# Kernel optimization log

Hardware: AMD Instinct MI355X
Metric: run time of the kernel (lower is better)

## Reference

```python
import jax, jax.numpy as jnp
import numpy as np


def _l2norm(x):
    # matches torch F.normalize(p=2, dim=-1) with eps clamp
    return x / jnp.clip(jnp.linalg.norm(x, axis=-1, keepdims=True), 1e-12)


def setup_inputs() -> dict:
    key = jax.random.key(0)
    k1, k2 = jax.random.split(key)
    I, J, S, H = 32, 32, 256, 768
    return {
        "query_embs": jax.random.normal(k1, (I, S, H), dtype=jnp.float32),
        "key_embs": jax.random.normal(k2, (J, S, H), dtype=jnp.float32),
        "q_mask": jnp.ones((I, S), dtype=jnp.float32),
        "k_mask": jnp.ones((J, S), dtype=jnp.float32),
        "alpha_raw": jnp.asarray(0.5, dtype=jnp.float32),  # learned scalar param
    }


def reference(query_embs, key_embs, q_mask, k_mask, alpha_raw):
    # eval path: gumbel_temp=None, use_max=False, do_distance=True, exp_decay=True
    S = query_embs.shape[1]
    pos = jnp.arange(S)
    distance = jnp.abs(pos[:, None] - pos[None, :]).astype(jnp.float32)  # [S, S]
    alpha = jax.nn.softplus(alpha_raw)

    qn = _l2norm(query_embs)  # [I, S, H]
    kn = _l2norm(key_embs)    # [J, T, H]

    # cross similarity [I, J, S, T] with exponential distance decay
    sim = jnp.einsum('ish,jth->ijst', qn, kn) * jnp.exp(-alpha * distance)

    # valid pair mask [I, J, S, T]
    valid = q_mask[:, None, :, None] * k_mask[None, :, None, :]
    masked = sim * valid - (1.0 - valid) * 1e9

    p = jax.nn.softmax(masked, axis=-1)             # softmax over key tokens t
    agg = jnp.einsum('ijst,jth->ijsh', p, kn)       # soft-aligned key embedding
    scores = jnp.einsum('ish,ijsh->ijs', qn, agg)   # per-query-token score
    scores = scores * q_mask[:, None, :]
    denom = jnp.clip(jnp.sum(q_mask, axis=-1, keepdims=True), 1.0)  # [I, 1]
    return jnp.sum(scores, axis=-1) / denom         # [I, J]
```

## Files before the change

### kernel.cpp

```cpp
#include <hip/hip_runtime.h>

#define I_DIM 32
#define J_DIM 32
#define S_DIM 256
#define H_DIM 768
#define KC    32
#define NCH   (H_DIM / KC)
#define TILE_B 32768
#define WSQ_BYTES ((size_t)I_DIM * NCH * TILE_B)
#define WSK_BYTES ((size_t)J_DIM * NCH * TILE_B)

typedef _Float16 f16x8 __attribute__((ext_vector_type(8)));
typedef float    f32x16 __attribute__((ext_vector_type(16)));

static __device__ __forceinline__ unsigned short f16bits(_Float16 h) {
    union { _Float16 f; unsigned short u; } cv; cv.f = h; return cv.u;
}

__global__ __launch_bounds__(256) void li_split_kernel(
    const float* __restrict__ qe, const float* __restrict__ ke,
    char* __restrict__ wsQ, char* __restrict__ wsK)
{
    const int lane = threadIdx.x & 63;
    const int w    = threadIdx.x >> 6;
    const int r    = blockIdx.x * 4 + w;
    const bool isQ = r < I_DIM * S_DIM;
    const int row  = isQ ? r : r - I_DIM * S_DIM;
    const float* base = (isQ ? qe : ke) + (size_t)row * H_DIM;

    float4 v[3];
    v[0] = *(const float4*)(base + 4 * lane);
    v[1] = *(const float4*)(base + 4 * lane + 256);
    v[2] = *(const float4*)(base + 4 * lane + 512);
    float ss = 0.0f;
    #pragma unroll
    for (int g = 0; g < 3; ++g)
        ss += v[g].x * v[g].x + v[g].y * v[g].y + v[g].z * v[g].z + v[g].w * v[g].w;
    #pragma unroll
    for (int m = 1; m < 64; m <<= 1) ss += __shfl_xor(ss, m, 64);
    const float inv = 1.0f / fmaxf(sqrtf(ss), 1e-12f);

    const int mi  = row >> 8;
    const int s   = row & 255;
    const int r7  = s & 7;
    char* wsb = (isQ ? wsQ : wsK) + (size_t)mi * NCH * TILE_B + s * 128;

    #pragma unroll
    for (int g = 0; g < 3; ++g) {
        const int k0 = 4 * lane + 256 * g;
        const int c  = k0 >> 5;
        const int kk = k0 & 31;
        float xn[4] = {v[g].x * inv, v[g].y * inv, v[g].z * inv, v[g].w * inv};
        unsigned short hb[4], lb[4];
        #pragma unroll
        for (int e = 0; e < 4; ++e) {
            _Float16 h  = (_Float16)xn[e];
            _Float16 lo = (_Float16)(xn[e] - (float)h);
            hb[e] = f16bits(h);
            lb[e] = f16bits(lo);
        }
        char* p = wsb + (size_t)c * TILE_B + (((kk >> 3) ^ r7) << 4) + (kk & 7) * 2;
        *(uint2*)(p)        = make_uint2(hb[0] | ((unsigned)hb[1] << 16), hb[2] | ((unsigned)hb[3] << 16));
        *(uint2*)((char*)((size_t)p ^ 64)) = make_uint2(lb[0] | ((unsigned)lb[1] << 16), lb[2] | ((unsigned)lb[3] << 16));
    }
}

__global__ __launch_bounds__(1024, 4) void li_mfma_kernel(
    const char* __restrict__ wsQ, const char* __restrict__ wsK,
    const float* __restrict__ qm, const float* __restrict__ km,
    const float* __restrict__ alpha_raw, float* __restrict__ out)
{
    __shared__ __align__(16) char sQ[2][TILE_B];
    __shared__ __align__(16) char sK[2][TILE_B];
    __shared__ float kmsh[256], qmsh[256];
    __shared__ float pm[256][4], pL[256][4], pW[256][4];
    __shared__ float redA[1024], redB[1024];

    const int tid = threadIdx.x;
    const int wid = tid >> 6;
    const int l   = tid & 63;
    const int l31 = l & 31;
    const int hi  = l >> 5;
    const int wx  = wid & 3;
    const int wy  = wid >> 2;
    const int r7  = l31 & 7;

    const int bidx = blockIdx.x;
    const int x  = bidx & 7;
    const int r0 = bidx >> 3;
    const int j  = x * 4 + (r0 & 3);
    const int i  = r0 >> 2;

    if (tid < 256) {
        kmsh[tid] = km[j * 256 + tid];
        qmsh[tid] = qm[i * 256 + tid];
    }
    const float araw  = alpha_raw[0];
    const float alpha = (araw > 20.0f) ? araw : log1pf(expf(araw));
    const float nal   = -alpha;

    const char* qbase = wsQ + (size_t)i * NCH * TILE_B;
    const char* kbase = wsK + (size_t)j * NCH * TILE_B;

    f32x16 acc[2][2];
    #pragma unroll
    for (int mr = 0; mr < 2; ++mr)
        #pragma unroll
        for (int nt = 0; nt < 2; ++nt)
            #pragma unroll
            for (int z = 0; z < 16; ++z) acc[mr][nt][z] = 0.0f;

#define STAGE(buf, c)                                                                      \
    do {                                                                                   \
        const char* qt_ = qbase + (size_t)(c) * TILE_B + wid * 2048 + l * 16;              \
        const char* kt_ = kbase + (size_t)(c) * TILE_B + wid * 2048 + l * 16;              \
        char* dq_ = sQ[buf] + wid * 2048;                                                  \
        char* dk_ = sK[buf] + wid * 2048;                                                  \
        _Pragma("unroll")                                                                  \
        for (int u = 0; u < 2; ++u)                                                        \
            __builtin_amdgcn_global_load_lds(                                              \
                (const __attribute__((address_space(1))) void*)(qt_ + u * 1024),           \
                (__attribute__((address_space(3))) void*)(dq_ + u * 1024), 16, 0, 0);      \
        _Pragma("unroll")                                                                  \
        for (int u = 0; u < 2; ++u)                                                        \
            __builtin_amdgcn_global_load_lds(                                              \
                (const __attribute__((address_space(1))) void*)(kt_ + u * 1024),           \
                (__attribute__((address_space(3))) void*)(dk_ + u * 1024), 16, 0, 0);      \
    } while (0)

    STAGE(0, 0);
    asm volatile("s_waitcnt vmcnt(0)" ::: "memory");
    __builtin_amdgcn_sched_barrier(0);
    __builtin_amdgcn_s_barrier();
    __builtin_amdgcn_sched_barrier(0);

    for (int c = 0; c < NCH; ++c) {
        if (c + 1 < NCH) {
            STAGE((c + 1) & 1, c + 1);
            asm volatile("s_waitcnt vmcnt(4)" ::: "memory");
        } else {
            asm volatile("s_waitcnt vmcnt(0)" ::: "memory");
        }
        __builtin_amdgcn_sched_barrier(0);
        __builtin_amdgcn_s_barrier();
        __builtin_amdgcn_sched_barrier(0);

        const char* bQ = sQ[c & 1];
        const char* bK = sK[c & 1];
        #pragma unroll
        for (int ks = 0; ks < 2; ++ks) {
            const int soff = ((ks * 2 + hi) ^ r7) << 4;
            const int rA = wy * 64 + l31;
            const int rB = rA + 32;
            const f16x8 qhA = *(const f16x8*)(bQ + rA * 128 + soff);
            const f16x8 qlA = *(const f16x8*)(bQ + ((rA * 128 + soff) ^ 64));
            const f16x8 qhB = *(const f16x8*)(bQ + rB * 128 + soff);
            const f16x8 qlB = *(const f16x8*)(bQ + ((rB * 128 + soff) ^ 64));
            const int c0 = wx * 64 + l31;
            const int c1 = c0 + 32;
            const f16x8 kh0 = *(const f16x8*)(bK + c0 * 128 + soff);
            const f16x8 kl0 = *(const f16x8*)(bK + ((c0 * 128 + soff) ^ 64));
            const f16x8 kh1 = *(const f16x8*)(bK + c1 * 128 + soff);
            const f16x8 kl1 = *(const f16x8*)(bK + ((c1 * 128 + soff) ^ 64));

            acc[0][0] = __builtin_amdgcn_mfma_f32_32x32x16_f16(qhA, kh0, acc[0][0], 0, 0, 0);
            acc[0][1] = __builtin_amdgcn_mfma_f32_32x32x16_f16(qhA, kh1, acc[0][1], 0, 0, 0);
            acc[1][0] = __builtin_amdgcn_mfma_f32_32x32x16_f16(qhB, kh0, acc[1][0], 0, 0, 0);
            acc[1][1] = __builtin_amdgcn_mfma_f32_32x32x16_f16(qhB, kh1, acc[1][1], 0, 0, 0);

            acc[0][0] = __builtin_amdgcn_mfma_f32_32x32x16_f16(qhA, kl0, acc[0][0], 0, 0, 0);
            acc[0][1] = __builtin_amdgcn_mfma_f32_32x32x16_f16(qhA, kl1, acc[0][1], 0, 0, 0);
            acc[1][0] = __builtin_amdgcn_mfma_f32_32x32x16_f16(qhB, kl0, acc[1][0], 0, 0, 0);
            acc[1][1] = __builtin_amdgcn_mfma_f32_32x32x16_f16(qhB, kl1, acc[1][1], 0, 0, 0);

            acc[0][0] = __builtin_amdgcn_mfma_f32_32x32x16_f16(qlA, kh0, acc[0][0], 0, 0, 0);
            acc[0][1] = __builtin_amdgcn_mfma_f32_32x32x16_f16(qlA, kh1, acc[0][1], 0, 0, 0);
            acc[1][0] = __builtin_amdgcn_mfma_f32_32x32x16_f16(qlB, kh0, acc[1][0], 0, 0, 0);
            acc[1][1] = __builtin_amdgcn_mfma_f32_32x32x16_f16(qlB, kh1, acc[1][1], 0, 0, 0);
        }
        __builtin_amdgcn_sched_barrier(0);
        __builtin_amdgcn_s_barrier();
        __builtin_amdgcn_sched_barrier(0);
    }
#undef STAGE

    #pragma unroll
    for (int mr = 0; mr < 2; ++mr) {
        #pragma unroll
        for (int z = 0; z < 16; ++z) {
            const int srow = wy * 64 + mr * 32 + hi * 4 + (z & 3) + 8 * (z >> 2);
            const float qms = qmsh[srow];
            float mv[2], cvv[2];
            float mloc = -3.0e38f;
            #pragma unroll
            for (int nt = 0; nt < 2; ++nt) {
                const int tcol = wx * 64 + nt * 32 + l31;
                const float cv = acc[mr][nt][z];
                int dd = srow - tcol; dd = dd < 0 ? -dd : dd;
                const float valid = qms * kmsh[tcol];
                const float m = cv * __expf(nal * (float)dd) * valid - (1.0f - valid) * 1e9f;
                mv[nt] = m; cvv[nt] = cv;
                mloc = fmaxf(mloc, m);
            }
            #pragma unroll
            for (int mm = 1; mm < 32; mm <<= 1)
                mloc = fmaxf(mloc, __shfl_xor(mloc, mm, 32));
            float L = 0.0f, W = 0.0f;
            #pragma unroll
            for (int nt = 0; nt < 2; ++nt) {
                const float e = __expf(mv[nt] - mloc);
                L += e;
                W += e * cvv[nt];
            }
            #pragma unroll
            for (int mm = 1; mm < 32; mm <<= 1) {
                L += __shfl_xor(L, mm, 32);
                W += __shfl_xor(W, mm, 32);
            }
            if (l31 == 0) {
                pm[srow][wx] = mloc;
                pL[srow][wx] = L;
                pW[srow][wx] = W;
            }
        }
    }
    __syncthreads();

    float contrib = 0.0f, qq = 0.0f;
    if (tid < 256) {
        float M = fmaxf(fmaxf(pm[tid][0], pm[tid][1]), fmaxf(pm[tid][2], pm[tid][3]));
        float L = 0.0f, W = 0.0f;
        #pragma unroll
        for (int q = 0; q < 4; ++q) {
            const float e = __expf(pm[tid][q] - M);
            L += pL[tid][q] * e;
            W += pW[tid][q] * e;
        }
        contrib = (W / L) * qmsh[tid];
        qq = qmsh[tid];
    }
    redA[tid] = contrib;
    redB[tid] = qq;
    __syncthreads();
    for (int off = 512; off > 0; off >>= 1) {
        if (tid < off) {
            redA[tid] += redA[tid + off];
            redB[tid] += redB[tid + off];
        }
        __syncthreads();
    }
    if (tid == 0) out[i * 32 + j] = redA[0] / fmaxf(redB[0], 1.0f);
}

extern "C" void kernel_launch(void* const* d_in, const int* in_sizes, int n_in,
                              void* d_out, int out_size, void* d_ws, size_t ws_size,
                              hipStream_t stream)
{
    const float* qe = (const float*)d_in[0];
    const float* ke = (const float*)d_in[1];
    const float* qm = (const float*)d_in[2];
    const float* km = (const float*)d_in[3];
    const float* al = (const float*)d_in[4];
    float* out = (float*)d_out;

    char* wsQ = (char*)d_ws;
    char* wsK = wsQ + WSQ_BYTES;

    hipLaunchKernelGGL(li_split_kernel, dim3((I_DIM + J_DIM) * S_DIM / 4), dim3(256),
                       0, stream, qe, ke, wsQ, wsK);
    hipLaunchKernelGGL(li_mfma_kernel, dim3(I_DIM * J_DIM), dim3(1024), 0, stream,
                       wsQ, wsK, qm, km, al, out);
}
```

Measured before the change: 441.1 us.

## Load K fragments directly from global into registers, stage only Q in LDS

```diff
diff --git a/kernel.cpp b/kernel.cpp
--- a/kernel.cpp
+++ b/kernel.cpp
@@ -4,8 +4,7 @@
 #define J_DIM 32
 #define S_DIM 256
 #define H_DIM 768
-#define KC    32
-#define NCH   (H_DIM / KC)
+#define NCH   24
 #define TILE_B 32768
 #define WSQ_BYTES ((size_t)I_DIM * NCH * TILE_B)
 #define WSK_BYTES ((size_t)J_DIM * NCH * TILE_B)
@@ -40,10 +39,9 @@
     for (int m = 1; m < 64; m <<= 1) ss += __shfl_xor(ss, m, 64);
     const float inv = 1.0f / fmaxf(sqrtf(ss), 1e-12f);
 
-    const int mi  = row >> 8;
-    const int s   = row & 255;
-    const int r7  = s & 7;
-    char* wsb = (isQ ? wsQ : wsK) + (size_t)mi * NCH * TILE_B + s * 128;
+    const int mi = row >> 8;
+    const int s  = row & 255;
+    const int r7 = s & 7;
 
     #pragma unroll
     for (int g = 0; g < 3; ++g) {
@@ -59,22 +57,31 @@
             hb[e] = f16bits(h);
             lb[e] = f16bits(lo);
         }
-        char* p = wsb + (size_t)c * TILE_B + (((kk >> 3) ^ r7) << 4) + (kk & 7) * 2;
-        *(uint2*)(p)        = make_uint2(hb[0] | ((unsigned)hb[1] << 16), hb[2] | ((unsigned)hb[3] << 16));
-        *(uint2*)((char*)((size_t)p ^ 64)) = make_uint2(lb[0] | ((unsigned)lb[1] << 16), lb[2] | ((unsigned)lb[3] << 16));
-    }
-}
-
-__global__ __launch_bounds__(1024, 4) void li_mfma_kernel(
+        const uint2 hv = make_uint2(hb[0] | ((unsigned)hb[1] << 16), hb[2] | ((unsigned)hb[3] << 16));
+        const uint2 lv = make_uint2(lb[0] | ((unsigned)lb[1] << 16), lb[2] | ((unsigned)lb[3] << 16));
+        if (isQ) {
+            char* p = wsQ + (size_t)mi * NCH * TILE_B + s * 128
+                    + (size_t)c * TILE_B + (((kk >> 3) ^ r7) << 4) + (kk & 7) * 2;
+            *(uint2*)p = hv;
+            *(uint2*)((char*)((size_t)p ^ 64)) = lv;
+        } else {
+            char* p = wsK + (size_t)mi * NCH * TILE_B
+                    + (size_t)c * TILE_B + (kk >> 3) * 8192 + s * 16 + (kk & 7) * 2;
+            *(uint2*)p = hv;
+            *(uint2*)(p + 4096) = lv;
+        }
+    }
+}
+
+__global__ __launch_bounds__(512, 2) void li_mfma_kernel(
     const char* __restrict__ wsQ, const char* __restrict__ wsK,
     const float* __restrict__ qm, const float* __restrict__ km,
     const float* __restrict__ alpha_raw, float* __restrict__ out)
 {
     __shared__ __align__(16) char sQ[2][TILE_B];
-    __shared__ __align__(16) char sK[2][TILE_B];
     __shared__ float kmsh[256], qmsh[256];
     __shared__ float pm[256][4], pL[256][4], pW[256][4];
-    __shared__ float redA[1024], redB[1024];
+    __shared__ float redA[512], redB[512];
 
     const int tid = threadIdx.x;
     const int wid = tid >> 6;
@@ -100,95 +107,103 @@
     const float nal   = -alpha;
 
     const char* qbase = wsQ + (size_t)i * NCH * TILE_B;
-    const char* kbase = wsK + (size_t)j * NCH * TILE_B;
-
-    f32x16 acc[2][2];
-    #pragma unroll
-    for (int mr = 0; mr < 2; ++mr)
+    const char* kcl = wsK + (size_t)j * NCH * TILE_B
+                    + (size_t)hi * 8192 + (size_t)(wx * 64 + l31) * 16;
+
+    f32x16 acc[4][2];
+    #pragma unroll
+    for (int mr = 0; mr < 4; ++mr)
         #pragma unroll
         for (int nt = 0; nt < 2; ++nt)
             #pragma unroll
             for (int z = 0; z < 16; ++z) acc[mr][nt][z] = 0.0f;
 
-#define STAGE(buf, c)                                                                      \
-    do {                                                                                   \
-        const char* qt_ = qbase + (size_t)(c) * TILE_B + wid * 2048 + l * 16;              \
-        const char* kt_ = kbase + (size_t)(c) * TILE_B + wid * 2048 + l * 16;              \
-        char* dq_ = sQ[buf] + wid * 2048;                                                  \
-        char* dk_ = sK[buf] + wid * 2048;                                                  \
-        _Pragma("unroll")                                                                  \
-        for (int u = 0; u < 2; ++u)                                                        \
-            __builtin_amdgcn_global_load_lds(                                              \
-                (const __attribute__((address_space(1))) void*)(qt_ + u * 1024),           \
-                (__attribute__((address_space(3))) void*)(dq_ + u * 1024), 16, 0, 0);      \
-        _Pragma("unroll")                                                                  \
-        for (int u = 0; u < 2; ++u)                                                        \
-            __builtin_amdgcn_global_load_lds(                                              \
-                (const __attribute__((address_space(1))) void*)(kt_ + u * 1024),           \
-                (__attribute__((address_space(3))) void*)(dk_ + u * 1024), 16, 0, 0);      \
-    } while (0)
-
-    STAGE(0, 0);
-    asm volatile("s_waitcnt vmcnt(0)" ::: "memory");
-    __builtin_amdgcn_sched_barrier(0);
-    __builtin_amdgcn_s_barrier();
-    __builtin_amdgcn_sched_barrier(0);
+    f16x8 qh[4], ql[4];
+    f16x8 ka0, ka1, kal0, kal1;
+    f16x8 kb0, kb1, kbl0, kbl1;
+
+#define KLOAD(H0, H1, L0, L1, c, ks)                                        \
+    do {                                                                    \
+        const char* a_ = kcl + (size_t)(c) * TILE_B + (ks) * 16384;         \
+        H0 = *(const f16x8*)(a_);                                           \
+        H1 = *(const f16x8*)(a_ + 512);                                     \
+        L0 = *(const f16x8*)(a_ + 4096);                                    \
+        L1 = *(const f16x8*)(a_ + 4608);                                    \
+    } while (0)
+
+#define QSTAGE(buf, c)                                                                 \
+    do {                                                                               \
+        const char* qt_ = qbase + (size_t)(c) * TILE_B + wid * 4096 + l * 16;          \
+        char* dq_ = sQ[buf] + wid * 4096;                                              \
+        _Pragma("unroll")                                                              \
+        for (int u = 0; u < 4; ++u)                                                    \
+            __builtin_amdgcn_global_load_lds(                                          \
+                (const __attribute__((address_space(1))) void*)(qt_ + u * 1024),       \
+                (__attribute__((address_space(3))) void*)(dq_ + u * 1024), 16, 0, 0);  \
+    } while (0)
+
+#define QREAD(bQ, ks)                                                       \
+    do {                                                                    \
+        const int soff_ = (((ks) * 2 + hi) ^ r7) << 4;                      \
+        _Pragma("unroll")                                                   \
+        for (int mr = 0; mr < 4; ++mr) {                                    \
+            const int rq_ = (wy * 128 + mr * 32 + l31) * 128;               \
+            qh[mr] = *(const f16x8*)((bQ) + rq_ + soff_);                   \
+            ql[mr] = *(const f16x8*)((bQ) + ((rq_ + soff_) ^ 64));          \
+        }                                                                   \
+    } while (0)
+
+#define MFMA1(A, B, C) __builtin_amdgcn_mfma_f32_32x32x16_f16(A, B, C, 0, 0, 0)
+#define MFMAS(KH0, KH1, KL0, KL1)                                           \
+    do {                                                                    \
+        _Pragma("unroll")                                                   \
+        for (int mr = 0; mr < 4; ++mr) {                                    \
+            acc[mr][0] = MFMA1(qh[mr], KH0, acc[mr][0]);                    \
+            acc[mr][1] = MFMA1(qh[mr], KH1, acc[mr][1]);                    \
+        }                                                                   \
+        _Pragma("unroll")                                                   \
+        for (int mr = 0; mr < 4; ++mr) {                                    \
+            acc[mr][0] = MFMA1(qh[mr], KL0, acc[mr][0]);                    \
+            acc[mr][1] = MFMA1(qh[mr], KL1, acc[mr][1]);                    \
+        }                                                                   \
+        _Pragma("unroll")                                                   \
+        for (int mr = 0; mr < 4; ++mr) {                                    \
+            acc[mr][0] = MFMA1(ql[mr], KH0, acc[mr][0]);                    \
+            acc[mr][1] = MFMA1(ql[mr], KH1, acc[mr][1]);                    \
+        }                                                                   \
+    } while (0)
+
+    QSTAGE(0, 0);
+    KLOAD(ka0, ka1, kal0, kal1, 0, 0);
 
     for (int c = 0; c < NCH; ++c) {
-        if (c + 1 < NCH) {
-            STAGE((c + 1) & 1, c + 1);
-            asm volatile("s_waitcnt vmcnt(4)" ::: "memory");
-        } else {
-            asm volatile("s_waitcnt vmcnt(0)" ::: "memory");
-        }
+        asm volatile("s_waitcnt vmcnt(0)" ::: "memory");
         __builtin_amdgcn_sched_barrier(0);
         __builtin_amdgcn_s_barrier();
         __builtin_amdgcn_sched_barrier(0);
 
         const char* bQ = sQ[c & 1];
-        const char* bK = sK[c & 1];
-        #pragma unroll
-        for (int ks = 0; ks < 2; ++ks) {
-            const int soff = ((ks * 2 + hi) ^ r7) << 4;
-            const int rA = wy * 64 + l31;
-            const int rB = rA + 32;
-            const f16x8 qhA = *(const f16x8*)(bQ + rA * 128 + soff);
-            const f16x8 qlA = *(const f16x8*)(bQ + ((rA * 128 + soff) ^ 64));
-            const f16x8 qhB = *(const f16x8*)(bQ + rB * 128 + soff);
-            const f16x8 qlB = *(const f16x8*)(bQ + ((rB * 128 + soff) ^ 64));
-            const int c0 = wx * 64 + l31;
-            const int c1 = c0 + 32;
-            const f16x8 kh0 = *(const f16x8*)(bK + c0 * 128 + soff);
-            const f16x8 kl0 = *(const f16x8*)(bK + ((c0 * 128 + soff) ^ 64));
-            const f16x8 kh1 = *(const f16x8*)(bK + c1 * 128 + soff);
-            const f16x8 kl1 = *(const f16x8*)(bK + ((c1 * 128 + soff) ^ 64));
-
-            acc[0][0] = __builtin_amdgcn_mfma_f32_32x32x16_f16(qhA, kh0, acc[0][0], 0, 0, 0);
-            acc[0][1] = __builtin_amdgcn_mfma_f32_32x32x16_f16(qhA, kh1, acc[0][1], 0, 0, 0);
-            acc[1][0] = __builtin_amdgcn_mfma_f32_32x32x16_f16(qhB, kh0, acc[1][0], 0, 0, 0);
-            acc[1][1] = __builtin_amdgcn_mfma_f32_32x32x16_f16(qhB, kh1, acc[1][1], 0, 0, 0);
-
-            acc[0][0] = __builtin_amdgcn_mfma_f32_32x32x16_f16(qhA, kl0, acc[0][0], 0, 0, 0);
-            acc[0][1] = __builtin_amdgcn_mfma_f32_32x32x16_f16(qhA, kl1, acc[0][1], 0, 0, 0);
-            acc[1][0] = __builtin_amdgcn_mfma_f32_32x32x16_f16(qhB, kl0, acc[1][0], 0, 0, 0);
-            acc[1][1] = __builtin_amdgcn_mfma_f32_32x32x16_f16(qhB, kl1, acc[1][1], 0, 0, 0);
-
-            acc[0][0] = __builtin_amdgcn_mfma_f32_32x32x16_f16(qlA, kh0, acc[0][0], 0, 0, 0);
-            acc[0][1] = __builtin_amdgcn_mfma_f32_32x32x16_f16(qlA, kh1, acc[0][1], 0, 0, 0);
-            acc[1][0] = __builtin_amdgcn_mfma_f32_32x32x16_f16(qlB, kh0, acc[1][0], 0, 0, 0);
-            acc[1][1] = __builtin_amdgcn_mfma_f32_32x32x16_f16(qlB, kh1, acc[1][1], 0, 0, 0);
-        }
-        __builtin_amdgcn_sched_barrier(0);
-        __builtin_amdgcn_s_barrier();
-        __builtin_amdgcn_sched_barrier(0);
-    }
-#undef STAGE
-
-    #pragma unroll
-    for (int mr = 0; mr < 2; ++mr) {
+        KLOAD(kb0, kb1, kbl0, kbl1, c, 1);
+        QREAD(bQ, 0);
+        MFMAS(ka0, ka1, kal0, kal1);
+        if (c + 1 < NCH) {
+            KLOAD(ka0, ka1, kal0, kal1, c + 1, 0);
+            QSTAGE((c + 1) & 1, c + 1);
+        }
+        QREAD(bQ, 1);
+        MFMAS(kb0, kb1, kbl0, kbl1);
+    }
+#undef KLOAD
+#undef QSTAGE
+#undef QREAD
+#undef MFMAS
+#undef MFMA1
+
+    #pragma unroll
+    for (int mr = 0; mr < 4; ++mr) {
         #pragma unroll
         for (int z = 0; z < 16; ++z) {
-            const int srow = wy * 64 + mr * 32 + hi * 4 + (z & 3) + 8 * (z >> 2);
+            const int srow = wy * 128 + mr * 32 + hi * 4 + (z & 3) + 8 * (z >> 2);
             const float qms = qmsh[srow];
             float mv[2], cvv[2];
             float mloc = -3.0e38f;
@@ -242,7 +257,7 @@
     redA[tid] = contrib;
     redB[tid] = qq;
     __syncthreads();
-    for (int off = 512; off > 0; off >>= 1) {
+    for (int off = 256; off > 0; off >>= 1) {
         if (tid < off) {
             redA[tid] += redA[tid + off];
             redB[tid] += redB[tid + off];
@@ -268,6 +283,6 @@
 
     hipLaunchKernelGGL(li_split_kernel, dim3((I_DIM + J_DIM) * S_DIM / 4), dim3(256),
                        0, stream, qe, ke, wsQ, wsK);
-    hipLaunchKernelGGL(li_mfma_kernel, dim3(I_DIM * J_DIM), dim3(1024), 0, stream,
+    hipLaunchKernelGGL(li_mfma_kernel, dim3(I_DIM * J_DIM), dim3(512), 0, stream,
                        wsQ, wsK, qm, km, al, out);
 }
```

After: 461.5 us. 4.6% more time.
